# Kernel tuning notes

Hardware: AMD Instinct MI355X
Metric: run time of the kernel (lower is better)

The kernel has to match this reference:

```python
import jax, jax.numpy as jnp
import numpy as np

C = 128
EPS = 1e-5


def _layernorm(x, w, b):
    m = jnp.mean(x, axis=-1, keepdims=True)
    v = jnp.mean(jnp.square(x - m), axis=-1, keepdims=True)
    return (x - m) * jax.lax.rsqrt(v + EPS) * w + b


def _linear(x, w, b):
    # torch Linear: y = x @ W.T + b, W is [out, in]
    return jnp.einsum('bijc,dc->bijd', x, w) + b


def setup_inputs() -> dict:
    key = jax.random.key(0)
    ks = jax.random.split(key, 8)
    B, N = 1, 384
    z = jax.random.normal(ks[0], (B, N, N, C), dtype=jnp.float32)
    pair_mask = jnp.ones((B, N, N), dtype=jnp.float32)
    def W(k):
        return jax.random.normal(k, (C, C), dtype=jnp.float32) * 0.02
    return {
        'z': z,
        'pair_mask': pair_mask,
        'ln_in_w': jnp.ones((C,), jnp.float32),
        'ln_in_b': jnp.zeros((C,), jnp.float32),
        'ln_out_w': jnp.ones((C,), jnp.float32),
        'ln_out_b': jnp.zeros((C,), jnp.float32),
        'proj_a_w': W(ks[1]), 'proj_a_b': jnp.zeros((C,), jnp.float32),
        'gate_a_w': W(ks[2]), 'gate_a_b': jnp.zeros((C,), jnp.float32),
        'proj_b_w': W(ks[3]), 'proj_b_b': jnp.zeros((C,), jnp.float32),
        'gate_b_w': W(ks[4]), 'gate_b_b': jnp.zeros((C,), jnp.float32),
        'gate_o_w': W(ks[5]), 'gate_o_b': jnp.zeros((C,), jnp.float32),
        'proj_o_w': W(ks[6]), 'proj_o_b': jnp.zeros((C,), jnp.float32),
    }


def reference(z, pair_mask, ln_in_w, ln_in_b, ln_out_w, ln_out_b,
              proj_a_w, proj_a_b, gate_a_w, gate_a_b,
              proj_b_w, proj_b_b, gate_b_w, gate_b_b,
              gate_o_w, gate_o_b, proj_o_w, proj_o_b):
    mask = pair_mask[..., None]                     # [B,N,N,1]
    z_norm = _layernorm(z, ln_in_w, ln_in_b)
    gate = jax.nn.sigmoid(_linear(z_norm, gate_o_w, gate_o_b))
    a = _linear(z_norm, proj_a_w, proj_a_b) * jax.nn.sigmoid(_linear(z_norm, gate_a_w, gate_a_b)) * mask
    b = _linear(z_norm, proj_b_w, proj_b_b) * jax.nn.sigmoid(_linear(z_norm, gate_b_w, gate_b_b)) * mask
    # incoming: out[i,j,c] = sum_k a[k,j,c] * b[k,i,c]
    contracted = jnp.einsum('bkjc,bkic->bijc', a, b)
    contracted = contracted * mask
    out = _linear(_layernorm(contracted, ln_out_w, ln_out_b), proj_o_w, proj_o_b)
    return out * gate
```

## Files before the change

### kernel.cpp

```cpp
#include <hip/hip_runtime.h>
#include <math.h>

#define NN 384
#define CC 128
#define MT (NN * NN)

typedef __attribute__((ext_vector_type(8))) short bf16x8;
typedef __attribute__((ext_vector_type(4))) short short4v;
typedef __attribute__((ext_vector_type(4))) float f32x4;

__device__ __forceinline__ float bf2f(short u) {
  union { float f; unsigned i; } v; v.i = ((unsigned)(unsigned short)u) << 16; return v.f;
}
__device__ __forceinline__ short f2bf(float f) {
  union { float f; unsigned i; } v; v.f = f;
  unsigned x = v.i;
  return (short)((x + 0x7fffu + ((x >> 16) & 1u)) >> 16);
}
__device__ __forceinline__ void cp16(void* lds, const void* g) {
  __builtin_amdgcn_global_load_lds(
      (const __attribute__((address_space(1))) void*)g,
      (__attribute__((address_space(3))) void*)lds, 16, 0, 0);
}
__device__ __forceinline__ float sigm(float x) { return 1.f / (1.f + __expf(-x)); }


__global__ __launch_bounds__(256) void k_wts(
    const float* __restrict__ w0, const float* __restrict__ w1,
    const float* __restrict__ w2, const float* __restrict__ w3,
    const float* __restrict__ w4, const float* __restrict__ w5,
    short* __restrict__ out)
{
  int idx = blockIdx.x * 256 + threadIdx.x;
  const float* s;
  switch (idx >> 14) {
    case 0: s = w0; break; case 1: s = w1; break; case 2: s = w2; break;
    case 3: s = w3; break; case 4: s = w4; break; default: s = w5; break;
  }
  out[idx] = f2bf(s[idx & 16383]);
}

__global__ __launch_bounds__(256) void k_ln_in(
    const float* __restrict__ z, const float* __restrict__ lw,
    const float* __restrict__ lb, short* __restrict__ zn)
{
  const int wid = threadIdx.x >> 6, lane = threadIdx.x & 63;
  const size_t p = (size_t)blockIdx.x * 4 + wid;
  const float2 v = ((const float2*)(z + p * CC))[lane];
  float s = v.x + v.y, sq = v.x * v.x + v.y * v.y;
  #pragma unroll
  for (int o = 32; o > 0; o >>= 1) { s += __shfl_xor(s, o); sq += __shfl_xor(sq, o); }
  const float mu = s * (1.f / 128.f);
  const float rstd = rsqrtf(sq * (1.f / 128.f) - mu * mu + 1e-5f);
  const float2 w2 = ((const float2*)lw)[lane];
  const float2 b2 = ((const float2*)lb)[lane];
  short2 o2;
  o2.x = f2bf((v.x - mu) * rstd * w2.x + b2.x);
  o2.y = f2bf((v.y - mu) * rstd * w2.y + b2.y);
  ((short2*)(zn + p * CC))[lane] = o2;
}

__global__ __launch_bounds__(256) void k_lin(
    const short* __restrict__ zn, const short* __restrict__ Bw,
    const float* __restrict__ bias_p, const float* __restrict__ bias_g,
    const float* __restrict__ mask, short* __restrict__ outp)
{
  __shared__ char smem[49152];
  __shared__ float mask_s[128];
  short* As = (short*)smem;
  short* Bs = (short*)(smem + 16384);
  short* T  = (short*)smem;

  const int tid = threadIdx.x, wid = tid >> 6, lane = tid & 63;
  const int tile = blockIdx.x;
  const int y0 = tile / 3, x0 = (tile % 3) * 128;

  if (tid < 128) mask_s[tid] = mask[(size_t)(x0 + tid) * NN + y0];

  f32x4 accP[4][4], accG[4][4];
  #pragma unroll
  for (int i = 0; i < 4; ++i) {
    #pragma unroll
    for (int j = 0; j < 4; ++j) {
      accP[i][j] = f32x4{0.f, 0.f, 0.f, 0.f};
      accG[i][j] = f32x4{0.f, 0.f, 0.f, 0.f};
    }
  }
  const int wm = (wid >> 1) * 64, wn = (wid & 1) * 64;
  const int slot = (lane & 7) ^ (lane >> 3);

  #pragma unroll
  for (int kk = 0; kk < 2; ++kk) {
    __syncthreads();
    #pragma unroll
    for (int i = 0; i < 4; ++i) {
      const int rbase = (i * 4 + wid) * 8;
      const int r = rbase + (lane >> 3);
      cp16((char*)As + rbase * 128,
           (const char*)(zn + ((size_t)(x0 + r) * NN + y0) * CC) + kk * 128 + slot * 16);
    }
    #pragma unroll
    for (int i = 0; i < 8; ++i) {
      const int rbase = (i * 4 + wid) * 8;
      const int r = rbase + (lane >> 3);
      cp16((char*)Bs + rbase * 128,
           (const char*)(Bw + (size_t)r * CC) + kk * 128 + slot * 16);
    }
    __syncthreads();
    #pragma unroll
    for (int ks = 0; ks < 2; ++ks) {
      const int u = ks * 4 + (lane >> 4);
      const int sl = (u ^ (lane & 7)) * 8;
      bf16x8 a[4], bp[4], bg[4];
      #pragma unroll
      for (int f = 0; f < 4; ++f) {
        a[f]  = *(const bf16x8*)&As[(wm + f * 16 + (lane & 15)) * 64 + sl];
        bp[f] = *(const bf16x8*)&Bs[(wn + f * 16 + (lane & 15)) * 64 + sl];
        bg[f] = *(const bf16x8*)&Bs[128 * 64 + (wn + f * 16 + (lane & 15)) * 64 + sl];
      }
      #pragma unroll
      for (int fm = 0; fm < 4; ++fm) {
        #pragma unroll
        for (int fn = 0; fn < 4; ++fn) {
          accP[fm][fn] = __builtin_amdgcn_mfma_f32_16x16x32_bf16(a[fm], bp[fn], accP[fm][fn], 0, 0, 0);
          accG[fm][fn] = __builtin_amdgcn_mfma_f32_16x16x32_bf16(a[fm], bg[fn], accG[fm][fn], 0, 0, 0);
        }
      }
    }
  }

  __syncthreads();
  #pragma unroll
  for (int fm = 0; fm < 4; ++fm) {
    #pragma unroll
    for (int fn = 0; fn < 4; ++fn) {
      const int c = wn + fn * 16 + (lane & 15);
      const int mb = wm + fm * 16 + (lane >> 4) * 4;
      const float bpv = bias_p[c];
      const float bgv = bias_g[c];
      short4v st;
      #pragma unroll
      for (int e = 0; e < 4; ++e) {
        const float pv = accP[fm][fn][e] + bpv;
        const float gv = accG[fm][fn][e] + bgv;
        st[e] = f2bf(pv * sigm(gv) * mask_s[mb + e]);
      }
      *(short4v*)&T[c * 136 + mb] = st;
    }
  }
  __syncthreads();
  const size_t rowoff = (size_t)y0 * NN + x0;
  #pragma unroll
  for (int rep = 0; rep < 8; ++rep) {
    const int row = rep * 16 + (tid >> 4), chunk = tid & 15;
    const bf16x8 v = *(const bf16x8*)&T[row * 136 + chunk * 8];
    *(bf16x8*)(outp + (size_t)row * MT + rowoff + chunk * 8) = v;
  }
}

__global__ __launch_bounds__(256) void k_tri(
    const short* __restrict__ wsa, const short* __restrict__ wsb,
    const float* __restrict__ mask, short* __restrict__ wsct)
{
  __shared__ char smem[34816];
  short* As = (short*)smem;
  short* Bs = (short*)(smem + 16384);
  short* T  = (short*)smem;

  const int tid = threadIdx.x, wid = tid >> 6, lane = tid & 63;
  const int o = (blockIdx.x & 7) * 144 + (blockIdx.x >> 3);
  const int c = o / 9, t9 = o % 9;
  const int i0 = (t9 / 3) * 128, j0 = (t9 % 3) * 128;
  const short* Ab = wsa + (size_t)c * MT;
  const short* Bb = wsb + (size_t)c * MT;

  f32x4 acc[4][4];
  #pragma unroll
  for (int i = 0; i < 4; ++i) {
    #pragma unroll
    for (int j = 0; j < 4; ++j) acc[i][j] = f32x4{0.f, 0.f, 0.f, 0.f};
  }
  const int wm = (wid >> 1) * 64, wn = (wid & 1) * 64;
  const int slot = (lane & 7) ^ (lane >> 3);

  for (int kt = 0; kt < 6; ++kt) {
    __syncthreads();
    #pragma unroll
    for (int i = 0; i < 4; ++i) {
      const int rbase = (i * 4 + wid) * 8;
      const int r = rbase + (lane >> 3);
      cp16((char*)As + rbase * 128,
           (const char*)(Ab + (size_t)(j0 + r) * NN) + kt * 128 + slot * 16);
      cp16((char*)Bs + rbase * 128,
           (const char*)(Bb + (size_t)(i0 + r) * NN) + kt * 128 + slot * 16);
    }
    __syncthreads();
    #pragma unroll
    for (int ks = 0; ks < 2; ++ks) {
      const int u = ks * 4 + (lane >> 4);
      const int sl = (u ^ (lane & 7)) * 8;
      bf16x8 a[4], b[4];
      #pragma unroll
      for (int f = 0; f < 4; ++f) {
        a[f] = *(const bf16x8*)&As[(wm + f * 16 + (lane & 15)) * 64 + sl];
        b[f] = *(const bf16x8*)&Bs[(wn + f * 16 + (lane & 15)) * 64 + sl];
      }
      #pragma unroll
      for (int fm = 0; fm < 4; ++fm) {
        #pragma unroll
        for (int fn = 0; fn < 4; ++fn)
          acc[fm][fn] = __builtin_amdgcn_mfma_f32_16x16x32_bf16(a[fm], b[fn], acc[fm][fn], 0, 0, 0);
      }
    }
  }

  __syncthreads();
  #pragma unroll
  for (int fm = 0; fm < 4; ++fm) {
    #pragma unroll
    for (int fn = 0; fn < 4; ++fn) {
      const int il = wn + fn * 16 + (lane & 15);
      const int jb = wm + fm * 16 + (lane >> 4) * 4;
      const f32x4 mk = *(const f32x4*)(mask + (size_t)(i0 + il) * NN + j0 + jb);
      short4v st;
      #pragma unroll
      for (int e = 0; e < 4; ++e) st[e] = f2bf(acc[fm][fn][e] * mk[e]);
      *(short4v*)&T[il * 136 + jb] = st;
    }
  }
  __syncthreads();
  #pragma unroll
  for (int rep = 0; rep < 8; ++rep) {
    const int row = rep * 16 + (tid >> 4), chunk = tid & 15;
    const bf16x8 v = *(const bf16x8*)&T[row * 136 + chunk * 8];
    *(bf16x8*)(wsct + (size_t)c * MT + (size_t)(i0 + row) * NN + j0 + chunk * 8) = v;
  }
}

__global__ __launch_bounds__(256) void k_fin(
    const short* __restrict__ wsct, const short* __restrict__ zn,
    const short* __restrict__ wpo, const short* __restrict__ wgo,
    const float* __restrict__ lw, const float* __restrict__ lb,
    const float* __restrict__ po_b, const float* __restrict__ go_b,
    float* __restrict__ out)
{
  __shared__ char smem[81920];
  short* Tt    = (short*)smem;
  float* lnw_s = (float*)(smem + 34816);
  float* lnb_s = (float*)(smem + 35328);
  short* As2   = (short*)smem;
  short* Bs    = (short*)(smem + 16384);
  short* A1    = (short*)(smem + 49152);

  const int tid = threadIdx.x, wid = tid >> 6, lane = tid & 63;
  const size_t p0 = (size_t)blockIdx.x * 128;

  #pragma unroll
  for (int rep = 0; rep < 8; ++rep) {
    const int c = rep * 16 + (tid >> 4), chunk = tid & 15;
    const bf16x8 v = *(const bf16x8*)(wsct + (size_t)c * MT + p0 + chunk * 8);
    *(bf16x8*)&Tt[c * 136 + chunk * 8] = v;
  }
  if (tid < 128) { lnw_s[tid] = lw[tid]; lnb_s[tid] = lb[tid]; }
  __syncthreads();

  const int pl = tid >> 1, q = tid & 1;
  float s = 0.f, sq = 0.f;
  #pragma unroll
  for (int cc = 0; cc < 64; ++cc) {
    const float v = bf2f(Tt[(q * 64 + cc) * 136 + pl]);
    s += v; sq += v * v;
  }
  s += __shfl_xor(s, 1); sq += __shfl_xor(sq, 1);
  const float mu = s * (1.f / 128.f);
  const float rstd = rsqrtf(sq * (1.f / 128.f) - mu * mu + 1e-5f);

  #pragma unroll
  for (int cb = 0; cb < 8; ++cb) {
    const int c0 = q * 64 + cb * 8;
    bf16x8 st;
    #pragma unroll
    for (int e = 0; e < 8; ++e) {
      const int c = c0 + e;
      st[e] = f2bf((bf2f(Tt[c * 136 + pl]) - mu) * rstd * lnw_s[c] + lnb_s[c]);
    }
    const int slotg = q * 8 + cb;
    const int kk = slotg >> 3, s3 = slotg & 7;
    *(bf16x8*)&A1[kk * 8192 + pl * 64 + (s3 ^ (pl & 7)) * 8] = st;
  }

  f32x4 accO[4][4], accG[4][4];
  #pragma unroll
  for (int i = 0; i < 4; ++i) {
    #pragma unroll
    for (int j = 0; j < 4; ++j) {
      accO[i][j] = f32x4{0.f, 0.f, 0.f, 0.f};
      accG[i][j] = f32x4{0.f, 0.f, 0.f, 0.f};
    }
  }
  const int wm = (wid >> 1) * 64, wn = (wid & 1) * 64;
  const int slot = (lane & 7) ^ (lane >> 3);

  #pragma unroll
  for (int kk = 0; kk < 2; ++kk) {
    __syncthreads();
    #pragma unroll
    for (int i = 0; i < 4; ++i) {
      const int rbase = (i * 4 + wid) * 8;
      const int r = rbase + (lane >> 3);
      cp16((char*)As2 + rbase * 128,
           (const char*)(zn + (p0 + r) * CC) + kk * 128 + slot * 16);
    }
    #pragma unroll
    for (int i = 0; i < 8; ++i) {
      const int rbase = (i * 4 + wid) * 8;
      const int r = rbase + (lane >> 3);
      const short* wrow = (r < 128) ? (wpo + (size_t)r * CC) : (wgo + (size_t)(r - 128) * CC);
      cp16((char*)Bs + rbase * 128, (const char*)wrow + kk * 128 + slot * 16);
    }
    __syncthreads();
    #pragma unroll
    for (int ks = 0; ks < 2; ++ks) {
      const int u = ks * 4 + (lane >> 4);
      const int sl = (u ^ (lane & 7)) * 8;
      bf16x8 a1[4], a2[4], bo[4], bg[4];
      #pragma unroll
      for (int f = 0; f < 4; ++f) {
        const int row = wm + f * 16 + (lane & 15);
        a1[f] = *(const bf16x8*)&A1[kk * 8192 + row * 64 + sl];
        a2[f] = *(const bf16x8*)&As2[row * 64 + sl];
      }
      #pragma unroll
      for (int f = 0; f < 4; ++f) {
        const int row = wn + f * 16 + (lane & 15);
        bo[f] = *(const bf16x8*)&Bs[row * 64 + sl];
        bg[f] = *(const bf16x8*)&Bs[(128 + row) * 64 + sl];
      }
      #pragma unroll
      for (int fm = 0; fm < 4; ++fm) {
        #pragma unroll
        for (int fn = 0; fn < 4; ++fn) {
          accO[fm][fn] = __builtin_amdgcn_mfma_f32_16x16x32_bf16(a1[fm], bo[fn], accO[fm][fn], 0, 0, 0);
          accG[fm][fn] = __builtin_amdgcn_mfma_f32_16x16x32_bf16(a2[fm], bg[fn], accG[fm][fn], 0, 0, 0);
        }
      }
    }
  }

  #pragma unroll
  for (int fm = 0; fm < 4; ++fm) {
    #pragma unroll
    for (int fn = 0; fn < 4; ++fn) {
      const int d = wn + fn * 16 + (lane & 15);
      const int mb = wm + fm * 16 + (lane >> 4) * 4;
      const float bd = po_b[d];
      const float gd = go_b[d];
      #pragma unroll
      for (int e = 0; e < 4; ++e) {
        const float g = sigm(accG[fm][fn][e] + gd);
        out[(p0 + mb + e) * CC + d] = (accO[fm][fn][e] + bd) * g;
      }
    }
  }
}

extern "C" void kernel_launch(void* const* d_in, const int* in_sizes, int n_in,
                              void* d_out, int out_size, void* d_ws, size_t ws_size,
                              hipStream_t stream) {
  const float* z        = (const float*)d_in[0];
  const float* mask     = (const float*)d_in[1];
  const float* ln_in_w  = (const float*)d_in[2];
  const float* ln_in_b  = (const float*)d_in[3];
  const float* ln_out_w = (const float*)d_in[4];
  const float* ln_out_b = (const float*)d_in[5];
  const float* pa_w = (const float*)d_in[6];  const float* pa_b = (const float*)d_in[7];
  const float* ga_w = (const float*)d_in[8];  const float* ga_b = (const float*)d_in[9];
  const float* pb_w = (const float*)d_in[10]; const float* pb_b = (const float*)d_in[11];
  const float* gb_w = (const float*)d_in[12]; const float* gb_b = (const float*)d_in[13];
  const float* go_w = (const float*)d_in[14]; const float* go_b = (const float*)d_in[15];
  const float* po_w = (const float*)d_in[16]; const float* po_b = (const float*)d_in[17];

  char* ws = (char*)d_ws;
  const size_t SZ = (size_t)MT * CC * 2;
  short* zn   = (short*)(ws);
  short* wsa  = (short*)(ws + SZ);
  short* wsb  = (short*)(ws + 2 * SZ);
  short* wsct = (short*)(ws + 3 * SZ);
  short* wts  = (short*)(ws + 4 * SZ);

  k_wts<<<384, 256, 0, stream>>>(pa_w, ga_w, pb_w, gb_w, go_w, po_w, wts);
  k_ln_in<<<MT / 4, 256, 0, stream>>>(z, ln_in_w, ln_in_b, zn);
  k_lin<<<1152, 256, 0, stream>>>(zn, wts,             pa_b, ga_b, mask, wsa);
  k_lin<<<1152, 256, 0, stream>>>(zn, wts + 2 * 16384, pb_b, gb_b, mask, wsb);
  k_tri<<<1152, 256, 0, stream>>>(wsa, wsb, mask, wsct);
  k_fin<<<1152, 256, 0, stream>>>(wsct, zn, wts + 5 * 16384, wts + 4 * 16384,
                                  ln_out_w, ln_out_b, po_b, go_b, (float*)d_out);
}
```

Before: 329.2 us.

## Fold output layernorm into projection epilogue and add transposed normalized input copy

The output layernorm's weight is folded into the output projection weights, and precomputed row sums let mean and rstd be applied in the GEMM epilogue, so normalized activations are no longer written per element. k_fin stages the contracted tile with async LDS copies and splits the two GEMMs so they need less shared memory. k_ln_in also writes a transposed copy of the normalized input, so k_lin reads contiguous rows instead of strided ones. The cost is an extra full-size bf16 write in k_ln_in, and precision shifts because the raw contracted values are used unnormalized in bf16.

```diff
diff --git a/kernel.cpp b/kernel.cpp
--- a/kernel.cpp
+++ b/kernel.cpp
@@ -29,23 +29,40 @@
     const float* __restrict__ w0, const float* __restrict__ w1,
     const float* __restrict__ w2, const float* __restrict__ w3,
     const float* __restrict__ w4, const float* __restrict__ w5,
-    short* __restrict__ out)
+    const float* __restrict__ lw, short* __restrict__ out)
 {
   int idx = blockIdx.x * 256 + threadIdx.x;
+  const int plane = idx >> 14, q = idx & 16383;
   const float* s;
-  switch (idx >> 14) {
+  switch (plane) {
     case 0: s = w0; break; case 1: s = w1; break; case 2: s = w2; break;
     case 3: s = w3; break; case 4: s = w4; break; default: s = w5; break;
   }
-  out[idx] = f2bf(s[idx & 16383]);
+  float v = s[q];
+  if (plane == 5) v *= lw[q & 127];
+  out[idx] = f2bf(v);
+}
+
+__global__ void k_const(const float* __restrict__ po_w, const float* __restrict__ lw,
+                        const float* __restrict__ lb, float* __restrict__ Sc)
+{
+  const int d = threadIdx.x;
+  float s1 = 0.f, s2 = 0.f;
+  for (int c = 0; c < 128; ++c) {
+    const float w = po_w[d * 128 + c];
+    s1 += lw[c] * w; s2 += lb[c] * w;
+  }
+  Sc[d] = s1; Sc[128 + d] = s2;
 }
 
 __global__ __launch_bounds__(256) void k_ln_in(
     const float* __restrict__ z, const float* __restrict__ lw,
-    const float* __restrict__ lb, short* __restrict__ zn)
+    const float* __restrict__ lb, short* __restrict__ zn, short* __restrict__ zn_t)
 {
   const int wid = threadIdx.x >> 6, lane = threadIdx.x & 63;
   const size_t p = (size_t)blockIdx.x * 4 + wid;
+  const int i = (int)(p / NN), j = (int)(p - (size_t)i * NN);
+  const size_t pT = (size_t)j * NN + i;
   const float2 v = ((const float2*)(z + p * CC))[lane];
   float s = v.x + v.y, sq = v.x * v.x + v.y * v.y;
   #pragma unroll
@@ -58,10 +75,11 @@
   o2.x = f2bf((v.x - mu) * rstd * w2.x + b2.x);
   o2.y = f2bf((v.y - mu) * rstd * w2.y + b2.y);
   ((short2*)(zn + p * CC))[lane] = o2;
+  ((short2*)(zn_t + pT * CC))[lane] = o2;
 }
 
 __global__ __launch_bounds__(256) void k_lin(
-    const short* __restrict__ zn, const short* __restrict__ Bw,
+    const short* __restrict__ znt, const short* __restrict__ Bw,
     const float* __restrict__ bias_p, const float* __restrict__ bias_g,
     const float* __restrict__ mask, short* __restrict__ outp)
 {
@@ -97,7 +115,7 @@
       const int rbase = (i * 4 + wid) * 8;
       const int r = rbase + (lane >> 3);
       cp16((char*)As + rbase * 128,
-           (const char*)(zn + ((size_t)(x0 + r) * NN + y0) * CC) + kk * 128 + slot * 16);
+           (const char*)(znt + ((size_t)y0 * NN + x0 + r) * CC) + kk * 128 + slot * 16);
     }
     #pragma unroll
     for (int i = 0; i < 8; ++i) {
@@ -239,56 +257,58 @@
 
 __global__ __launch_bounds__(256) void k_fin(
     const short* __restrict__ wsct, const short* __restrict__ zn,
-    const short* __restrict__ wpo, const short* __restrict__ wgo,
-    const float* __restrict__ lw, const float* __restrict__ lb,
-    const float* __restrict__ po_b, const float* __restrict__ go_b,
-    float* __restrict__ out)
-{
-  __shared__ char smem[81920];
-  short* Tt    = (short*)smem;
-  float* lnw_s = (float*)(smem + 34816);
-  float* lnb_s = (float*)(smem + 35328);
-  short* As2   = (short*)smem;
-  short* Bs    = (short*)(smem + 16384);
-  short* A1    = (short*)(smem + 49152);
-
-  const int tid = threadIdx.x, wid = tid >> 6, lane = tid & 63;
+    const short* __restrict__ wpo , const short* __restrict__ wgo,
+    const float* __restrict__ Sc, const float* __restrict__ po_b,
+    const float* __restrict__ go_b, float* __restrict__ out)
+{
+  __shared__ char smem[68608];
+  short*  Tt   = (short*)smem;
+  short*  St   = (short*)smem;
+  short*  A1   = (short*)(smem + 32768);
+  float2* part = (float2*)(smem + 65536);
+  float*  muS  = (float*)(smem + 65536 + 2048);
+  float*  rsS  = (float*)(smem + 65536 + 2048 + 512);
+
+  const int tid = threadIdx.x, w = tid >> 6, lane = tid & 63;
   const size_t p0 = (size_t)blockIdx.x * 128;
-
-  #pragma unroll
-  for (int rep = 0; rep < 8; ++rep) {
-    const int c = rep * 16 + (tid >> 4), chunk = tid & 15;
-    const bf16x8 v = *(const bf16x8*)(wsct + (size_t)c * MT + p0 + chunk * 8);
-    *(bf16x8*)&Tt[c * 136 + chunk * 8] = v;
-  }
-  if (tid < 128) { lnw_s[tid] = lw[tid]; lnb_s[tid] = lb[tid]; }
-  __syncthreads();
-
-  const int pl = tid >> 1, q = tid & 1;
-  float s = 0.f, sq = 0.f;
-  #pragma unroll
-  for (int cc = 0; cc < 64; ++cc) {
-    const float v = bf2f(Tt[(q * 64 + cc) * 136 + pl]);
-    s += v; sq += v * v;
-  }
-  s += __shfl_xor(s, 1); sq += __shfl_xor(sq, 1);
-  const float mu = s * (1.f / 128.f);
-  const float rstd = rsqrtf(sq * (1.f / 128.f) - mu * mu + 1e-5f);
-
-  #pragma unroll
-  for (int cb = 0; cb < 8; ++cb) {
-    const int c0 = q * 64 + cb * 8;
-    bf16x8 st;
-    #pragma unroll
-    for (int e = 0; e < 8; ++e) {
-      const int c = c0 + e;
-      st[e] = f2bf((bf2f(Tt[c * 136 + pl]) - mu) * rstd * lnw_s[c] + lnb_s[c]);
-    }
-    const int slotg = q * 8 + cb;
-    const int kk = slotg >> 3, s3 = slotg & 7;
-    *(bf16x8*)&A1[kk * 8192 + pl * 64 + (s3 ^ (pl & 7)) * 8] = st;
-  }
-
+  const int slot = (lane & 7) ^ (lane >> 3);
+
+  #pragma unroll
+  for (int i = 0; i < 8; ++i) {
+    const int r0 = (i * 4 + w) * 4 + (lane >> 4);
+    cp16((char*)Tt + (i * 4 + w) * 1024 + (lane & 48) * 16,
+         (const char*)(wsct + (size_t)r0 * MT + p0) + (lane & 15) * 16);
+  }
+  __syncthreads();
+
+  {
+    const int pl = ((w & 1) << 6) | lane;
+    const int q  = w >> 1;
+    float s = 0.f, sq = 0.f;
+    #pragma unroll
+    for (int cb = 0; cb < 8; ++cb) {
+      bf16x8 st;
+      #pragma unroll
+      for (int e = 0; e < 8; ++e) {
+        const short u = Tt[(q * 64 + cb * 8 + e) * 128 + pl];
+        const float f = bf2f(u);
+        s += f; sq += f * f;
+        st[e] = u;
+      }
+      *(bf16x8*)&A1[q * 8192 + pl * 64 + ((cb ^ (pl & 7)) << 3)] = st;
+    }
+    part[q * 128 + pl] = float2{s, sq};
+  }
+  __syncthreads();
+  if (tid < 128) {
+    const float2 a = part[tid], b = part[128 + tid];
+    const float S = a.x + b.x, Q = a.y + b.y;
+    const float mu = S * (1.f / 128.f);
+    muS[tid] = mu;
+    rsS[tid] = rsqrtf(Q * (1.f / 128.f) - mu * mu + 1e-5f);
+  }
+
+  const int wm = (w >> 1) * 64, wn = (w & 1) * 64;
   f32x4 accO[4][4], accG[4][4];
   #pragma unroll
   for (int i = 0; i < 4; ++i) {
@@ -298,51 +318,64 @@
       accG[i][j] = f32x4{0.f, 0.f, 0.f, 0.f};
     }
   }
-  const int wm = (wid >> 1) * 64, wn = (wid & 1) * 64;
-  const int slot = (lane & 7) ^ (lane >> 3);
 
   #pragma unroll
   for (int kk = 0; kk < 2; ++kk) {
     __syncthreads();
     #pragma unroll
     for (int i = 0; i < 4; ++i) {
-      const int rbase = (i * 4 + wid) * 8;
+      const int rbase = (i * 4 + w) * 8;
       const int r = rbase + (lane >> 3);
-      cp16((char*)As2 + rbase * 128,
-           (const char*)(zn + (p0 + r) * CC) + kk * 128 + slot * 16);
-    }
-    #pragma unroll
-    for (int i = 0; i < 8; ++i) {
-      const int rbase = (i * 4 + wid) * 8;
-      const int r = rbase + (lane >> 3);
-      const short* wrow = (r < 128) ? (wpo + (size_t)r * CC) : (wgo + (size_t)(r - 128) * CC);
-      cp16((char*)Bs + rbase * 128, (const char*)wrow + kk * 128 + slot * 16);
+      cp16((char*)St + rbase * 128, (const char*)(wpo + (size_t)r * CC) + kk * 128 + slot * 16);
     }
     __syncthreads();
     #pragma unroll
     for (int ks = 0; ks < 2; ++ks) {
       const int u = ks * 4 + (lane >> 4);
       const int sl = (u ^ (lane & 7)) * 8;
-      bf16x8 a1[4], a2[4], bo[4], bg[4];
+      bf16x8 a[4], b[4];
       #pragma unroll
       for (int f = 0; f < 4; ++f) {
-        const int row = wm + f * 16 + (lane & 15);
-        a1[f] = *(const bf16x8*)&A1[kk * 8192 + row * 64 + sl];
-        a2[f] = *(const bf16x8*)&As2[row * 64 + sl];
-      }
-      #pragma unroll
-      for (int f = 0; f < 4; ++f) {
-        const int row = wn + f * 16 + (lane & 15);
-        bo[f] = *(const bf16x8*)&Bs[row * 64 + sl];
-        bg[f] = *(const bf16x8*)&Bs[(128 + row) * 64 + sl];
+        a[f] = *(const bf16x8*)&A1[kk * 8192 + (wm + f * 16 + (lane & 15)) * 64 + sl];
+        b[f] = *(const bf16x8*)&St[(wn + f * 16 + (lane & 15)) * 64 + sl];
       }
       #pragma unroll
       for (int fm = 0; fm < 4; ++fm) {
         #pragma unroll
-        for (int fn = 0; fn < 4; ++fn) {
-          accO[fm][fn] = __builtin_amdgcn_mfma_f32_16x16x32_bf16(a1[fm], bo[fn], accO[fm][fn], 0, 0, 0);
-          accG[fm][fn] = __builtin_amdgcn_mfma_f32_16x16x32_bf16(a2[fm], bg[fn], accG[fm][fn], 0, 0, 0);
-        }
+        for (int fn = 0; fn < 4; ++fn)
+          accO[fm][fn] = __builtin_amdgcn_mfma_f32_16x16x32_bf16(a[fm], b[fn], accO[fm][fn], 0, 0, 0);
+      }
+    }
+  }
+
+  #pragma unroll
+  for (int kk = 0; kk < 2; ++kk) {
+    __syncthreads();
+    #pragma unroll
+    for (int i = 0; i < 4; ++i) {
+      const int rbase = (i * 4 + w) * 8;
+      const int r = rbase + (lane >> 3);
+      cp16((char*)St + rbase * 128,
+           (const char*)(zn + (p0 + r) * CC) + kk * 128 + slot * 16);
+      cp16((char*)St + 16384 + rbase * 128,
+           (const char*)(wgo + (size_t)r * CC) + kk * 128 + slot * 16);
+    }
+    __syncthreads();
+    #pragma unroll
+    for (int ks = 0; ks < 2; ++ks) {
+      const int u = ks * 4 + (lane >> 4);
+      const int sl = (u ^ (lane & 7)) * 8;
+      bf16x8 a[4], b[4];
+      #pragma unroll
+      for (int f = 0; f < 4; ++f) {
+        a[f] = *(const bf16x8*)&St[(wm + f * 16 + (lane & 15)) * 64 + sl];
+        b[f] = *(const bf16x8*)&St[8192 + (wn + f * 16 + (lane & 15)) * 64 + sl];
+      }
+      #pragma unroll
+      for (int fm = 0; fm < 4; ++fm) {
+        #pragma unroll
+        for (int fn = 0; fn < 4; ++fn)
+          accG[fm][fn] = __builtin_amdgcn_mfma_f32_16x16x32_bf16(a[fm], b[fn], accG[fm][fn], 0, 0, 0);
       }
     }
   }
@@ -353,12 +386,14 @@
     for (int fn = 0; fn < 4; ++fn) {
       const int d = wn + fn * 16 + (lane & 15);
       const int mb = wm + fm * 16 + (lane >> 4) * 4;
-      const float bd = po_b[d];
-      const float gd = go_b[d];
+      const float S1 = Sc[d], S2 = Sc[128 + d];
+      const float bd = po_b[d], gd = go_b[d];
       #pragma unroll
       for (int e = 0; e < 4; ++e) {
+        const int pl = mb + e;
+        const float o = rsS[pl] * (accO[fm][fn][e] - muS[pl] * S1) + S2 + bd;
         const float g = sigm(accG[fm][fn][e] + gd);
-        out[(p0 + mb + e) * CC + d] = (accO[fm][fn][e] + bd) * g;
+        out[(p0 + pl) * CC + d] = o * g;
       }
     }
   }
@@ -383,16 +418,19 @@
   char* ws = (char*)d_ws;
   const size_t SZ = (size_t)MT * CC * 2;
   short* zn   = (short*)(ws);
-  short* wsa  = (short*)(ws + SZ);
-  short* wsb  = (short*)(ws + 2 * SZ);
-  short* wsct = (short*)(ws + 3 * SZ);
-  short* wts  = (short*)(ws + 4 * SZ);
-
-  k_wts<<<384, 256, 0, stream>>>(pa_w, ga_w, pb_w, gb_w, go_w, po_w, wts);
-  k_ln_in<<<MT / 4, 256, 0, stream>>>(z, ln_in_w, ln_in_b, zn);
-  k_lin<<<1152, 256, 0, stream>>>(zn, wts,             pa_b, ga_b, mask, wsa);
-  k_lin<<<1152, 256, 0, stream>>>(zn, wts + 2 * 16384, pb_b, gb_b, mask, wsb);
+  short* zn_t = (short*)(ws + SZ);
+  short* wsa  = (short*)(ws + 2 * SZ);
+  short* wsb  = (short*)(ws + 3 * SZ);
+  short* wsct = (short*)(ws + 4 * SZ);
+  short* wts  = (short*)(ws + 5 * SZ);
+  float* Sc   = (float*)(ws + 5 * SZ + 6 * 16384 * 2);
+
+  k_wts<<<384, 256, 0, stream>>>(pa_w, ga_w, pb_w, gb_w, go_w, po_w, ln_out_w, wts);
+  k_const<<<1, 128, 0, stream>>>(po_w, ln_out_w, ln_out_b, Sc);
+  k_ln_in<<<MT / 4, 256, 0, stream>>>(z, ln_in_w, ln_in_b, zn, zn_t);
+  k_lin<<<1152, 256, 0, stream>>>(zn_t, wts,             pa_b, ga_b, mask, wsa);
+  k_lin<<<1152, 256, 0, stream>>>(zn_t, wts + 2 * 16384, pb_b, gb_b, mask, wsb);
   k_tri<<<1152, 256, 0, stream>>>(wsa, wsb, mask, wsct);
   k_fin<<<1152, 256, 0, stream>>>(wsct, zn, wts + 5 * 16384, wts + 4 * 16384,
-                                  ln_out_w, ln_out_b, po_b, go_b, (float*)d_out);
-}
+                                  Sc, po_b, go_b, (float*)d_out);
+}
```

New measurement: 340.1 us. +3.3%, slower.

## Fold output LayerNorm into projection epilogue and double-buffer triangle GEMM

Applied to the files above, without the earlier changes.

The output LayerNorm weight is folded into the bf16 output-projection weights. Its mean and rstd are applied in the GEMM epilogue using precomputed column sums of W·lw and W·lb, so normalized activations no longer have to be written out. The triangle-multiplication kernel now double-buffers its LDS tiles so the next k-tile load overlaps the current MFMA work. The final kernel uses 64-row tiles (twice as many blocks) and reads weights and zn operands straight from global memory instead of staging them in LDS. The MFMA A operand is now the unnormalized bf16 contraction, which may lose some precision, and k_tri's LDS use doubles to 64 KB, which may lower occupancy.

```diff
diff --git a/kernel.cpp b/kernel.cpp
--- a/kernel.cpp
+++ b/kernel.cpp
@@ -29,15 +29,34 @@
     const float* __restrict__ w0, const float* __restrict__ w1,
     const float* __restrict__ w2, const float* __restrict__ w3,
     const float* __restrict__ w4, const float* __restrict__ w5,
-    short* __restrict__ out)
+    const float* __restrict__ lw, short* __restrict__ out)
 {
   int idx = blockIdx.x * 256 + threadIdx.x;
+  const int plane = idx >> 14, q = idx & 16383;
   const float* s;
-  switch (idx >> 14) {
+  switch (plane) {
     case 0: s = w0; break; case 1: s = w1; break; case 2: s = w2; break;
     case 3: s = w3; break; case 4: s = w4; break; default: s = w5; break;
   }
-  out[idx] = f2bf(s[idx & 16383]);
+  float v = s[q];
+  if (plane == 5) v *= lw[q & 127];
+  out[idx] = f2bf(v);
+}
+
+__global__ void k_const(const float* __restrict__ po_w, const float* __restrict__ lw,
+                        const float* __restrict__ lb, float* __restrict__ Sc)
+{
+  const int d = blockIdx.x, lane = threadIdx.x;
+  float s1 = 0.f, s2 = 0.f;
+  #pragma unroll
+  for (int c0 = 0; c0 < 128; c0 += 64) {
+    const int c = c0 + lane;
+    const float w = po_w[d * 128 + c];
+    s1 += lw[c] * w; s2 += lb[c] * w;
+  }
+  #pragma unroll
+  for (int o = 32; o > 0; o >>= 1) { s1 += __shfl_xor(s1, o); s2 += __shfl_xor(s2, o); }
+  if (lane == 0) { Sc[d] = s1; Sc[128 + d] = s2; }
 }
 
 __global__ __launch_bounds__(256) void k_ln_in(
@@ -162,10 +181,8 @@
     const short* __restrict__ wsa, const short* __restrict__ wsb,
     const float* __restrict__ mask, short* __restrict__ wsct)
 {
-  __shared__ char smem[34816];
-  short* As = (short*)smem;
-  short* Bs = (short*)(smem + 16384);
-  short* T  = (short*)smem;
+  __shared__ char smem[65536];
+  short* T = (short*)smem;
 
   const int tid = threadIdx.x, wid = tid >> 6, lane = tid & 63;
   const int o = (blockIdx.x & 7) * 144 + (blockIdx.x >> 3);
@@ -183,18 +200,26 @@
   const int wm = (wid >> 1) * 64, wn = (wid & 1) * 64;
   const int slot = (lane & 7) ^ (lane >> 3);
 
+  #define STAGE(kt, buf) { \
+    char* base = smem + (buf) * 32768; \
+    _Pragma("unroll") \
+    for (int i = 0; i < 4; ++i) { \
+      const int rbase = (i * 4 + wid) * 8; \
+      const int r = rbase + (lane >> 3); \
+      cp16(base + rbase * 128, \
+           (const char*)(Ab + (size_t)(j0 + r) * NN) + (kt) * 128 + slot * 16); \
+      cp16(base + 16384 + rbase * 128, \
+           (const char*)(Bb + (size_t)(i0 + r) * NN) + (kt) * 128 + slot * 16); \
+    } }
+
+  STAGE(0, 0);
+  __syncthreads();
+  #pragma unroll
   for (int kt = 0; kt < 6; ++kt) {
-    __syncthreads();
-    #pragma unroll
-    for (int i = 0; i < 4; ++i) {
-      const int rbase = (i * 4 + wid) * 8;
-      const int r = rbase + (lane >> 3);
-      cp16((char*)As + rbase * 128,
-           (const char*)(Ab + (size_t)(j0 + r) * NN) + kt * 128 + slot * 16);
-      cp16((char*)Bs + rbase * 128,
-           (const char*)(Bb + (size_t)(i0 + r) * NN) + kt * 128 + slot * 16);
-    }
-    __syncthreads();
+    const int buf = kt & 1;
+    if (kt < 5) STAGE(kt + 1, buf ^ 1);
+    short* As = (short*)(smem + buf * 32768);
+    short* Bs = (short*)(smem + buf * 32768 + 16384);
     #pragma unroll
     for (int ks = 0; ks < 2; ++ks) {
       const int u = ks * 4 + (lane >> 4);
@@ -212,9 +237,10 @@
           acc[fm][fn] = __builtin_amdgcn_mfma_f32_16x16x32_bf16(a[fm], b[fn], acc[fm][fn], 0, 0, 0);
       }
     }
-  }
-
-  __syncthreads();
+    __syncthreads();
+  }
+  #undef STAGE
+
   #pragma unroll
   for (int fm = 0; fm < 4; ++fm) {
     #pragma unroll
@@ -239,105 +265,86 @@
 
 __global__ __launch_bounds__(256) void k_fin(
     const short* __restrict__ wsct, const short* __restrict__ zn,
-    const short* __restrict__ wpo, const short* __restrict__ wgo,
-    const float* __restrict__ lw, const float* __restrict__ lb,
-    const float* __restrict__ po_b, const float* __restrict__ go_b,
-    float* __restrict__ out)
-{
-  __shared__ char smem[81920];
-  short* Tt    = (short*)smem;
-  float* lnw_s = (float*)(smem + 34816);
-  float* lnb_s = (float*)(smem + 35328);
-  short* As2   = (short*)smem;
-  short* Bs    = (short*)(smem + 16384);
-  short* A1    = (short*)(smem + 49152);
-
-  const int tid = threadIdx.x, wid = tid >> 6, lane = tid & 63;
-  const size_t p0 = (size_t)blockIdx.x * 128;
-
-  #pragma unroll
-  for (int rep = 0; rep < 8; ++rep) {
-    const int c = rep * 16 + (tid >> 4), chunk = tid & 15;
-    const bf16x8 v = *(const bf16x8*)(wsct + (size_t)c * MT + p0 + chunk * 8);
-    *(bf16x8*)&Tt[c * 136 + chunk * 8] = v;
-  }
-  if (tid < 128) { lnw_s[tid] = lw[tid]; lnb_s[tid] = lb[tid]; }
-  __syncthreads();
-
-  const int pl = tid >> 1, q = tid & 1;
-  float s = 0.f, sq = 0.f;
-  #pragma unroll
-  for (int cc = 0; cc < 64; ++cc) {
-    const float v = bf2f(Tt[(q * 64 + cc) * 136 + pl]);
-    s += v; sq += v * v;
-  }
-  s += __shfl_xor(s, 1); sq += __shfl_xor(sq, 1);
-  const float mu = s * (1.f / 128.f);
-  const float rstd = rsqrtf(sq * (1.f / 128.f) - mu * mu + 1e-5f);
-
-  #pragma unroll
-  for (int cb = 0; cb < 8; ++cb) {
-    const int c0 = q * 64 + cb * 8;
-    bf16x8 st;
-    #pragma unroll
-    for (int e = 0; e < 8; ++e) {
-      const int c = c0 + e;
-      st[e] = f2bf((bf2f(Tt[c * 136 + pl]) - mu) * rstd * lnw_s[c] + lnb_s[c]);
-    }
-    const int slotg = q * 8 + cb;
-    const int kk = slotg >> 3, s3 = slotg & 7;
-    *(bf16x8*)&A1[kk * 8192 + pl * 64 + (s3 ^ (pl & 7)) * 8] = st;
-  }
-
-  f32x4 accO[4][4], accG[4][4];
+    const short* __restrict__ wpo , const short* __restrict__ wgo,
+    const float* __restrict__ Sc, const float* __restrict__ po_b,
+    const float* __restrict__ go_b, float* __restrict__ out)
+{
+  __shared__ char smem[35328];
+  short*  Tt   = (short*)smem;
+  short*  A1   = (short*)(smem + 16384);
+  float2* part = (float2*)(smem + 32768);
+  float*  muS  = (float*)(smem + 34816);
+  float*  rsS  = (float*)(smem + 35072);
+
+  const int tid = threadIdx.x, w = tid >> 6, lane = tid & 63;
+  const size_t p0 = (size_t)blockIdx.x * 64;
+
   #pragma unroll
   for (int i = 0; i < 4; ++i) {
+    const int r = (i * 4 + w) * 8 + (lane >> 3);
+    cp16((char*)Tt + (i * 4 + w) * 1024,
+         (const char*)(wsct + (size_t)r * MT + p0) + (lane & 7) * 16);
+  }
+  __syncthreads();
+
+  {
+    const int pl = tid & 63, q = tid >> 6;
+    float s = 0.f, sq = 0.f;
+    #pragma unroll
+    for (int cb = 0; cb < 4; ++cb) {
+      bf16x8 st;
+      #pragma unroll
+      for (int e = 0; e < 8; ++e) {
+        const short u = Tt[(q * 32 + cb * 8 + e) * 64 + pl];
+        const float f = bf2f(u);
+        s += f; sq += f * f;
+        st[e] = u;
+      }
+      const int slot = (q & 1) * 4 + cb;
+      *(bf16x8*)&A1[(q >> 1) * 4096 + pl * 64 + ((slot ^ (pl & 7)) << 3)] = st;
+    }
+    part[q * 64 + pl] = float2{s, sq};
+  }
+  __syncthreads();
+  if (tid < 64) {
+    const float2 a = part[tid], b = part[64 + tid], c2 = part[128 + tid], d2 = part[192 + tid];
+    const float S = a.x + b.x + c2.x + d2.x, Q = a.y + b.y + c2.y + d2.y;
+    const float mu = S * (1.f / 128.f);
+    muS[tid] = mu;
+    rsS[tid] = rsqrtf(Q * (1.f / 128.f) - mu * mu + 1e-5f);
+  }
+  __syncthreads();
+
+  const int wm = (w >> 1) * 32, wn = (w & 1) * 64;
+  f32x4 accO[2][4], accG[2][4];
+  #pragma unroll
+  for (int i = 0; i < 2; ++i) {
     #pragma unroll
     for (int j = 0; j < 4; ++j) {
       accO[i][j] = f32x4{0.f, 0.f, 0.f, 0.f};
       accG[i][j] = f32x4{0.f, 0.f, 0.f, 0.f};
     }
   }
-  const int wm = (wid >> 1) * 64, wn = (wid & 1) * 64;
-  const int slot = (lane & 7) ^ (lane >> 3);
-
   #pragma unroll
   for (int kk = 0; kk < 2; ++kk) {
-    __syncthreads();
-    #pragma unroll
-    for (int i = 0; i < 4; ++i) {
-      const int rbase = (i * 4 + wid) * 8;
-      const int r = rbase + (lane >> 3);
-      cp16((char*)As2 + rbase * 128,
-           (const char*)(zn + (p0 + r) * CC) + kk * 128 + slot * 16);
-    }
-    #pragma unroll
-    for (int i = 0; i < 8; ++i) {
-      const int rbase = (i * 4 + wid) * 8;
-      const int r = rbase + (lane >> 3);
-      const short* wrow = (r < 128) ? (wpo + (size_t)r * CC) : (wgo + (size_t)(r - 128) * CC);
-      cp16((char*)Bs + rbase * 128, (const char*)wrow + kk * 128 + slot * 16);
-    }
-    __syncthreads();
     #pragma unroll
     for (int ks = 0; ks < 2; ++ks) {
       const int u = ks * 4 + (lane >> 4);
-      const int sl = (u ^ (lane & 7)) * 8;
-      bf16x8 a1[4], a2[4], bo[4], bg[4];
-      #pragma unroll
-      for (int f = 0; f < 4; ++f) {
+      bf16x8 a1[2], a2[2], bo[4], bg[4];
+      #pragma unroll
+      for (int f = 0; f < 2; ++f) {
         const int row = wm + f * 16 + (lane & 15);
-        a1[f] = *(const bf16x8*)&A1[kk * 8192 + row * 64 + sl];
-        a2[f] = *(const bf16x8*)&As2[row * 64 + sl];
+        a1[f] = *(const bf16x8*)&A1[kk * 4096 + row * 64 + ((u ^ (lane & 7)) << 3)];
+        a2[f] = *(const bf16x8*)(zn + (p0 + row) * CC + kk * 64 + u * 8);
       }
       #pragma unroll
       for (int f = 0; f < 4; ++f) {
         const int row = wn + f * 16 + (lane & 15);
-        bo[f] = *(const bf16x8*)&Bs[row * 64 + sl];
-        bg[f] = *(const bf16x8*)&Bs[(128 + row) * 64 + sl];
-      }
-      #pragma unroll
-      for (int fm = 0; fm < 4; ++fm) {
+        bo[f] = *(const bf16x8*)(wpo + (size_t)row * CC + kk * 64 + u * 8);
+        bg[f] = *(const bf16x8*)(wgo + (size_t)row * CC + kk * 64 + u * 8);
+      }
+      #pragma unroll
+      for (int fm = 0; fm < 2; ++fm) {
         #pragma unroll
         for (int fn = 0; fn < 4; ++fn) {
           accO[fm][fn] = __builtin_amdgcn_mfma_f32_16x16x32_bf16(a1[fm], bo[fn], accO[fm][fn], 0, 0, 0);
@@ -348,17 +355,19 @@
   }
 
   #pragma unroll
-  for (int fm = 0; fm < 4; ++fm) {
+  for (int fm = 0; fm < 2; ++fm) {
     #pragma unroll
     for (int fn = 0; fn < 4; ++fn) {
       const int d = wn + fn * 16 + (lane & 15);
       const int mb = wm + fm * 16 + (lane >> 4) * 4;
-      const float bd = po_b[d];
-      const float gd = go_b[d];
+      const float S1 = Sc[d], S2 = Sc[128 + d];
+      const float bd = po_b[d], gd = go_b[d];
       #pragma unroll
       for (int e = 0; e < 4; ++e) {
+        const int pl = mb + e;
+        const float o = rsS[pl] * (accO[fm][fn][e] - muS[pl] * S1) + S2 + bd;
         const float g = sigm(accG[fm][fn][e] + gd);
-        out[(p0 + mb + e) * CC + d] = (accO[fm][fn][e] + bd) * g;
+        out[(p0 + pl) * CC + d] = o * g;
       }
     }
   }
@@ -387,12 +396,14 @@
   short* wsb  = (short*)(ws + 2 * SZ);
   short* wsct = (short*)(ws + 3 * SZ);
   short* wts  = (short*)(ws + 4 * SZ);
-
-  k_wts<<<384, 256, 0, stream>>>(pa_w, ga_w, pb_w, gb_w, go_w, po_w, wts);
+  float* Sc   = (float*)(ws + 4 * SZ + 6 * 16384 * 2);
+
+  k_wts<<<384, 256, 0, stream>>>(pa_w, ga_w, pb_w, gb_w, go_w, po_w, ln_out_w, wts);
+  k_const<<<128, 64, 0, stream>>>(po_w, ln_out_w, ln_out_b, Sc);
   k_ln_in<<<MT / 4, 256, 0, stream>>>(z, ln_in_w, ln_in_b, zn);
   k_lin<<<1152, 256, 0, stream>>>(zn, wts,             pa_b, ga_b, mask, wsa);
   k_lin<<<1152, 256, 0, stream>>>(zn, wts + 2 * 16384, pb_b, gb_b, mask, wsb);
   k_tri<<<1152, 256, 0, stream>>>(wsa, wsb, mask, wsct);
-  k_fin<<<1152, 256, 0, stream>>>(wsct, zn, wts + 5 * 16384, wts + 4 * 16384,
-                                  ln_out_w, ln_out_b, po_b, go_b, (float*)d_out);
-}
+  k_fin<<<2304, 256, 0, stream>>>(wsct, zn, wts + 5 * 16384, wts + 4 * 16384,
+                                  Sc, po_b, go_b, (float*)d_out);
+}
```

Result: slower. 344.0 us (+4.5%).
